# Kernel optimization log

Hardware: AMD Instinct MI355X
Metric: run time of the kernel (lower is better)

The kernel has to match this reference:

```python
import jax, jax.numpy as jnp
import numpy as np

EPS = 1e-12  # F.normalize eps


def setup_inputs() -> dict:
    key = jax.random.key(0)
    k1, k2, k3, k4 = jax.random.split(key, 4)
    D, K, H, W = 256, 64, 512, 512
    x = jax.random.normal(k1, (1, D, H, W), dtype=jnp.float32)
    c = jax.random.normal(k2, (K, D), dtype=jnp.float32)
    conv_w = jax.random.normal(k3, (K, D), dtype=jnp.float32) * (1.0 / np.sqrt(D))
    conv_b = jax.random.normal(k4, (K,), dtype=jnp.float32) * 0.01
    return {"x": x, "c": c, "conv_w": conv_w, "conv_b": conv_b}


def reference(x, c, conv_w, conv_b):
    # x: (1, D, H, W); base_cnn treated as identity (feature map given directly)
    _, D, H, W = x.shape
    K = conv_w.shape[0]
    N = H * W
    xf = x.reshape(D, N)                                  # (D, N) local descriptors

    # 1x1 conv soft-assignment: logits (K, N), softmax over clusters K
    logits = jnp.einsum('kd,dn->kn', conv_w, xf) + conv_b[:, None]
    a_bar = jax.nn.softmax(logits, axis=0)                # (K, N)

    # VLAD core (vectorized): V[k] = sum_n a_bar[k,n] * (x[:,n] - c[k])
    V = jnp.einsum('kn,dn->kd', a_bar, xf) - c * a_bar.sum(axis=1, keepdims=True)  # (K, D)

    # intra-normalization over cluster axis (dim=0), then per-row L2 (F.normalize default dim=1)
    V = V / jnp.maximum(jnp.linalg.norm(V, axis=0, keepdims=True), EPS)
    y = V / jnp.maximum(jnp.linalg.norm(V, axis=1, keepdims=True), EPS)
    return y
```

## Files before the change

kernel.cpp:

```cpp
#include <hip/hip_runtime.h>
#include <hip/hip_bf16.h>

#define DD    256
#define KK    64
#define NPIX  262144
#define NW    512
#define NWIN  2
#define GRID  256
#define BLOCK 1024

#define W_S   264
#define AB_S  520
#define XC_S  40
#define SV_S  129

typedef __attribute__((ext_vector_type(8))) short bf16x8;
typedef __attribute__((ext_vector_type(4))) float f32x4;

union Frag { bf16x8 v; int i[4]; };

__device__ __forceinline__ int cvtpk(float a, float b) {
    __hip_bfloat162 h = __float22bfloat162_rn(float2{a, b});
    int r; __builtin_memcpy(&r, &h, 4); return r;
}

__device__ __forceinline__ void lds_barrier() {
    asm volatile("s_waitcnt lgkmcnt(0)" ::: "memory");
    __builtin_amdgcn_s_barrier();
}

__global__ __launch_bounds__(BLOCK, 4)
void netvlad_fused(const float* __restrict__ x, const float* __restrict__ conv_w,
                   const float* __restrict__ conv_b, float* __restrict__ Vpart,
                   float* __restrict__ asum_part)
{
    __shared__ short Wl[KK * W_S];
    __shared__ short Ab[KK * AB_S];
    __shared__ union {
        short slice[16 * 32 * XC_S];
        float sv[KK * SV_S];
    } U2;

    const int t    = threadIdx.x;
    const int lane = t & 63;
    const int w    = t >> 6;
    const int l15  = lane & 15;
    const int q    = (lane >> 4) & 3;
    const int bid  = blockIdx.x;
    const size_t n0 = (size_t)bid * (NWIN * NW);

    const int dg = lane >> 3;
    const int ng = lane & 7;
    const size_t nself0 = n0 + 32 * w + 4 * ng;
    const size_t nself1 = n0 + NW + 32 * w + 4 * ng;

    float4 pr[2][4];
    #pragma unroll
    for (int j = 0; j < 4; ++j)
        pr[0][j] = *(const float4*)(x + (size_t)(4 * dg + j) * NPIX + nself0);
    __builtin_amdgcn_sched_barrier(0);

    #pragma unroll
    for (int i = 0; i < 16; ++i) {
        int idx = t + BLOCK * i;
        float wv = conv_w[idx];
        __hip_bfloat16 hb = __float2bfloat16(wv);
        short s; __builtin_memcpy(&s, &hb, 2);
        Wl[(idx >> 8) * W_S + (idx & 255)] = s;
    }

    #pragma unroll
    for (int j = 0; j < 4; ++j)
        pr[1][j] = *(const float4*)(x + (size_t)(32 + 4 * dg + j) * NPIX + nself0);
    __builtin_amdgcn_sched_barrier(0);

    lds_barrier();

    float asumReg = 0.f;
    f32x4 acc[4];
    #pragma unroll
    for (int ct = 0; ct < 4; ++ct) acc[ct] = (f32x4){0.f, 0.f, 0.f, 0.f};

    short* slice = &U2.slice[w * (32 * XC_S)];

    #pragma unroll
    for (int win = 0; win < NWIN; ++win) {
        const size_t nwin   = n0 + (size_t)win * NW;
        const size_t nselfw = nwin + 32 * w + 4 * ng;

        f32x4 Lc[2][4];
        #pragma unroll
        for (int nt = 0; nt < 2; ++nt)
            #pragma unroll
            for (int mt = 0; mt < 4; ++mt)
                Lc[nt][mt] = (f32x4){0.f, 0.f, 0.f, 0.f};

        #pragma unroll
        for (int ch = 0; ch < 8; ++ch) {
            const int cur = ch & 1;

            {
                const float* r0 = (const float*)&pr[cur][0];
                const float* r1 = (const float*)&pr[cur][1];
                const float* r2 = (const float*)&pr[cur][2];
                const float* r3 = (const float*)&pr[cur][3];
                #pragma unroll
                for (int c = 0; c < 4; ++c) {
                    int2 pk; pk.x = cvtpk(r0[c], r1[c]); pk.y = cvtpk(r2[c], r3[c]);
                    *(int2*)&slice[(4 * ng + c) * XC_S + 4 * dg] = pk;
                }
            }

            if (ch < 6) {
                #pragma unroll
                for (int j = 0; j < 4; ++j)
                    pr[cur][j] = *(const float4*)(x + (size_t)(32 * (ch + 2) + 4 * dg + j) * NPIX + nselfw);
                __builtin_amdgcn_sched_barrier(0);
            }

            Frag Bv[2];
            #pragma unroll
            for (int nt = 0; nt < 2; ++nt)
                Bv[nt] = *(const Frag*)&slice[(16 * nt + l15) * XC_S + 8 * q];
            #pragma unroll
            for (int mt = 0; mt < 4; ++mt) {
                Frag A = *(const Frag*)&Wl[(16 * mt + l15) * W_S + 32 * ch + 8 * q];
                #pragma unroll
                for (int nt = 0; nt < 2; ++nt)
                    Lc[nt][mt] = __builtin_amdgcn_mfma_f32_16x16x32_bf16(A.v, Bv[nt].v, Lc[nt][mt], 0, 0, 0);
            }
        }

        float breg[4][4];
        #pragma unroll
        for (int mt = 0; mt < 4; ++mt)
            #pragma unroll
            for (int r = 0; r < 4; ++r)
                breg[mt][r] = conv_b[16 * mt + 4 * q + r];

        #pragma unroll
        for (int nt = 0; nt < 2; ++nt) {
            float mx = -1e30f;
            #pragma unroll
            for (int mt = 0; mt < 4; ++mt)
                #pragma unroll
                for (int r = 0; r < 4; ++r) {
                    Lc[nt][mt][r] += breg[mt][r];
                    mx = fmaxf(mx, Lc[nt][mt][r]);
                }
            mx = fmaxf(mx, __shfl_xor(mx, 16));
            mx = fmaxf(mx, __shfl_xor(mx, 32));
            float s = 0.f;
            #pragma unroll
            for (int mt = 0; mt < 4; ++mt)
                #pragma unroll
                for (int r = 0; r < 4; ++r) {
                    float e = __expf(Lc[nt][mt][r] - mx);
                    Lc[nt][mt][r] = e;
                    s += e;
                }
            s += __shfl_xor(s, 16);
            s += __shfl_xor(s, 32);
            float inv = 1.0f / s;
            #pragma unroll
            for (int mt = 0; mt < 4; ++mt)
                #pragma unroll
                for (int r = 0; r < 4; ++r)
                    Lc[nt][mt][r] *= inv;
        }

        {
            float* buf = (float*)(U2.slice + w * (32 * XC_S));
            #pragma unroll
            for (int mt = 0; mt < 4; ++mt)
                #pragma unroll
                for (int r = 0; r < 4; ++r) {
                    float v = Lc[0][mt][r] + Lc[1][mt][r];
                    v += __shfl_xor(v, 1);
                    v += __shfl_xor(v, 2);
                    v += __shfl_xor(v, 4);
                    v += __shfl_xor(v, 8);
                    if (l15 == 0) buf[16 * mt + 4 * q + r] = v;
                }
        }

        #pragma unroll
        for (int nt = 0; nt < 2; ++nt)
            #pragma unroll
            for (int mt = 0; mt < 4; ++mt)
                #pragma unroll
                for (int r = 0; r < 4; ++r) {
                    __hip_bfloat16 hb = __float2bfloat16(Lc[nt][mt][r]);
                    short s; __builtin_memcpy(&s, &hb, 2);
                    Ab[(16 * mt + 4 * q + r) * AB_S + 32 * w + 16 * nt + l15] = s;
                }

        const float* xroww = x + (size_t)(16 * w + l15) * NPIX + nwin + 8 * q;
        float4 pv[4][2];
        #pragma unroll
        for (int d = 0; d < 4; ++d) {
            pv[d][0] = *(const float4*)(xroww + 32 * d);
            pv[d][1] = *(const float4*)(xroww + 32 * d + 4);
        }
        __builtin_amdgcn_sched_barrier(0);

        if (win == 0) {
            #pragma unroll
            for (int j = 0; j < 4; ++j)
                pr[0][j] = *(const float4*)(x + (size_t)(4 * dg + j) * NPIX + nself1);
            #pragma unroll
            for (int j = 0; j < 4; ++j)
                pr[1][j] = *(const float4*)(x + (size_t)(32 + 4 * dg + j) * NPIX + nself1);
            __builtin_amdgcn_sched_barrier(0);
        }

        lds_barrier();

        if (t < KK) {
            float s = 0.f;
            #pragma unroll
            for (int ww = 0; ww < 16; ++ww)
                s += ((const float*)(U2.slice + ww * (32 * XC_S)))[t];
            asumReg += s;
        }

        #pragma unroll
        for (int s = 0; s < 16; ++s) {
            const int cur = s & 3;
            Frag Af;
            Af.i[0] = cvtpk(pv[cur][0].x, pv[cur][0].y);
            Af.i[1] = cvtpk(pv[cur][0].z, pv[cur][0].w);
            Af.i[2] = cvtpk(pv[cur][1].x, pv[cur][1].y);
            Af.i[3] = cvtpk(pv[cur][1].z, pv[cur][1].w);
            if (s < 12) {
                pv[cur][0] = *(const float4*)(xroww + 32 * (s + 4));
                pv[cur][1] = *(const float4*)(xroww + 32 * (s + 4) + 4);
                __builtin_amdgcn_sched_barrier(0);
            }
            Frag Bf[4];
            #pragma unroll
            for (int ct = 0; ct < 4; ++ct)
                Bf[ct] = *(const Frag*)&Ab[(16 * ct + l15) * AB_S + 32 * s + 8 * q];
            #pragma unroll
            for (int ct = 0; ct < 4; ++ct)
                acc[ct] = __builtin_amdgcn_mfma_f32_16x16x32_bf16(Af.v, Bf[ct].v, acc[ct], 0, 0, 0);
        }

        if (win == 0)
            lds_barrier();
    }

    if (t < KK) asum_part[(size_t)bid * KK + t] = asumReg;

    float* vout = Vpart + (size_t)bid * (KK * DD);
    #pragma unroll
    for (int H = 0; H < 2; ++H) {
        __syncthreads();
        if ((w >> 3) == H) {
            #pragma unroll
            for (int ct = 0; ct < 4; ++ct)
                #pragma unroll
                for (int r = 0; r < 4; ++r) {
                    int k  = 16 * ct + l15;
                    int dl = 16 * w + 4 * q + r - 128 * H;
                    U2.sv[k * SV_S + dl] = acc[ct][r];
                }
        }
        __syncthreads();
        #pragma unroll
        for (int i = 0; i < 8; ++i) {
            int idx = t + BLOCK * i;
            int k = idx >> 7, dl = idx & 127;
            vout[k * DD + 128 * H + dl] = U2.sv[k * SV_S + dl];
        }
    }
}

__global__ __launch_bounds__(256)
void netvlad_reduce(const float* __restrict__ Vpart, const float* __restrict__ asum_part,
                    float* __restrict__ Vred, float* __restrict__ asum_red)
{
    __shared__ float sbuf[256];
    const int t = threadIdx.x;
    if (blockIdx.x < 256) {
        const int o = blockIdx.x * 64 + (t & 63);
        const int g = t >> 6;
        float s = 0.f;
        #pragma unroll 8
        for (int i = 0; i < 64; ++i)
            s += Vpart[(size_t)(g * 64 + i) * (KK * DD) + o];
        sbuf[t] = s;
        __syncthreads();
        if (t < 64) Vred[o] = sbuf[t] + sbuf[t + 64] + sbuf[t + 128] + sbuf[t + 192];
    } else {
        const int k = t & 63;
        const int g = t >> 6;
        float s = 0.f;
        #pragma unroll 8
        for (int i = 0; i < 64; ++i)
            s += asum_part[(size_t)(g * 64 + i) * KK + k];
        sbuf[t] = s;
        __syncthreads();
        if (t < 64) asum_red[k] = sbuf[t] + sbuf[t + 64] + sbuf[t + 128] + sbuf[t + 192];
    }
}

__global__ __launch_bounds__(1024)
void netvlad_finalize(const float* __restrict__ Vws, const float* __restrict__ asum_ws,
                      const float* __restrict__ c, float* __restrict__ y)
{
    __shared__ float sV[KK * DD];
    __shared__ float sa[KK];
    __shared__ float colf[DD];
    __shared__ float rowf[KK];
    const int t = threadIdx.x;

    if (t < KK) sa[t] = asum_ws[t];
    __syncthreads();

    #pragma unroll
    for (int i = 0; i < 16; ++i) {
        int idx = t + 1024 * i;
        sV[idx] = Vws[idx] - c[idx] * sa[idx >> 8];
    }
    __syncthreads();

    if (t < DD) {
        float s = 0.f;
        for (int k = 0; k < KK; ++k) { float v = sV[k * DD + t]; s += v * v; }
        colf[t] = 1.0f / fmaxf(sqrtf(s), 1e-12f);
    }
    __syncthreads();

    #pragma unroll
    for (int i = 0; i < 16; ++i) {
        int idx = t + 1024 * i;
        sV[idx] *= colf[idx & 255];
    }
    __syncthreads();

    {
        int k = t >> 4, p = t & 15;
        float s = 0.f;
        #pragma unroll
        for (int j = 0; j < 16; ++j) { float v = sV[k * DD + p + 16 * j]; s += v * v; }
        s += __shfl_xor(s, 1);
        s += __shfl_xor(s, 2);
        s += __shfl_xor(s, 4);
        s += __shfl_xor(s, 8);
        if (p == 0) rowf[k] = 1.0f / fmaxf(sqrtf(s), 1e-12f);
    }
    __syncthreads();

    #pragma unroll
    for (int i = 0; i < 16; ++i) {
        int idx = t + 1024 * i;
        y[idx] = sV[idx] * rowf[idx >> 8];
    }
}

extern "C" void kernel_launch(void* const* d_in, const int* in_sizes, int n_in,
                              void* d_out, int out_size, void* d_ws, size_t ws_size,
                              hipStream_t stream) {
    const float* x      = (const float*)d_in[0];
    const float* c      = (const float*)d_in[1];
    const float* conv_w = (const float*)d_in[2];
    const float* conv_b = (const float*)d_in[3];
    float* y = (float*)d_out;

    float* Vpart     = (float*)d_ws;
    float* asum_part = Vpart + (size_t)GRID * KK * DD;
    float* Vred      = asum_part + (size_t)GRID * KK;
    float* asum_red  = Vred + KK * DD;

    netvlad_fused<<<GRID, BLOCK, 0, stream>>>(x, conv_w, conv_b, Vpart, asum_part);
    netvlad_reduce<<<257, 256, 0, stream>>>(Vpart, asum_part, Vred, asum_red);
    netvlad_finalize<<<1, 1024, 0, stream>>>(Vred, asum_red, c, y);
}
```

Baseline: 101.4 us.

## Split waves into producer/consumer roles with double-buffered soft-assignment tiles

Waves 0-7 now compute logits and softmax for a 256-pixel window, and waves 8-15 accumulate the VLAD product for the previous window out of a double-buffered Ab tile. The intent is to overlap the assignment GEMM and softmax with the aggregation GEMM, where before each wave ran both phases in sequence with barriers between them. Each window now costs one barrier instead of two serialized phases. In exchange, consumer waves hold twice as many accumulators and the pipeline takes one extra fill step. The two halves may also be unequal in work, which would leave some waves idle.

```diff
diff --git a/kernel.cpp b/kernel.cpp
--- a/kernel.cpp
+++ b/kernel.cpp
@@ -4,13 +4,13 @@
 #define DD    256
 #define KK    64
 #define NPIX  262144
-#define NW    512
-#define NWIN  2
+#define NW    256
+#define NWIN  4
 #define GRID  256
 #define BLOCK 1024
 
 #define W_S   264
-#define AB_S  520
+#define AB_S  264
 #define XC_S  40
 #define SV_S  129
 
@@ -35,9 +35,10 @@
                    float* __restrict__ asum_part)
 {
     __shared__ short Wl[KK * W_S];
-    __shared__ short Ab[KK * AB_S];
+    __shared__ short Ab[2][KK * AB_S];
+    __shared__ float asb[2][8][KK];
     __shared__ union {
-        short slice[16 * 32 * XC_S];
+        short slice[8 * 32 * XC_S];
         float sv[KK * SV_S];
     } U2;
 
@@ -49,16 +50,20 @@
     const int bid  = blockIdx.x;
     const size_t n0 = (size_t)bid * (NWIN * NW);
 
+    const bool producer = (w < 8);
+    const int  cw = w - 8;
+
     const int dg = lane >> 3;
     const int ng = lane & 7;
     const size_t nself0 = n0 + 32 * w + 4 * ng;
-    const size_t nself1 = n0 + NW + 32 * w + 4 * ng;
 
     float4 pr[2][4];
-    #pragma unroll
-    for (int j = 0; j < 4; ++j)
-        pr[0][j] = *(const float4*)(x + (size_t)(4 * dg + j) * NPIX + nself0);
-    __builtin_amdgcn_sched_barrier(0);
+    if (producer) {
+        #pragma unroll
+        for (int j = 0; j < 4; ++j)
+            pr[0][j] = *(const float4*)(x + (size_t)(4 * dg + j) * NPIX + nself0);
+        __builtin_amdgcn_sched_barrier(0);
+    }
 
     #pragma unroll
     for (int i = 0; i < 16; ++i) {
@@ -69,207 +74,220 @@
         Wl[(idx >> 8) * W_S + (idx & 255)] = s;
     }
 
-    #pragma unroll
-    for (int j = 0; j < 4; ++j)
-        pr[1][j] = *(const float4*)(x + (size_t)(32 + 4 * dg + j) * NPIX + nself0);
-    __builtin_amdgcn_sched_barrier(0);
+    if (producer) {
+        #pragma unroll
+        for (int j = 0; j < 4; ++j)
+            pr[1][j] = *(const float4*)(x + (size_t)(32 + 4 * dg + j) * NPIX + nself0);
+        __builtin_amdgcn_sched_barrier(0);
+    }
+
+    f32x4 acc[2][4];
+    #pragma unroll
+    for (int rg = 0; rg < 2; ++rg)
+        #pragma unroll
+        for (int ct = 0; ct < 4; ++ct)
+            acc[rg][ct] = (f32x4){0.f, 0.f, 0.f, 0.f};
+    float asumReg = 0.f;
 
     lds_barrier();
 
-    float asumReg = 0.f;
-    f32x4 acc[4];
-    #pragma unroll
-    for (int ct = 0; ct < 4; ++ct) acc[ct] = (f32x4){0.f, 0.f, 0.f, 0.f};
-
-    short* slice = &U2.slice[w * (32 * XC_S)];
-
-    #pragma unroll
-    for (int win = 0; win < NWIN; ++win) {
-        const size_t nwin   = n0 + (size_t)win * NW;
-        const size_t nselfw = nwin + 32 * w + 4 * ng;
-
-        f32x4 Lc[2][4];
-        #pragma unroll
-        for (int nt = 0; nt < 2; ++nt)
-            #pragma unroll
-            for (int mt = 0; mt < 4; ++mt)
-                Lc[nt][mt] = (f32x4){0.f, 0.f, 0.f, 0.f};
-
-        #pragma unroll
-        for (int ch = 0; ch < 8; ++ch) {
-            const int cur = ch & 1;
-
-            {
-                const float* r0 = (const float*)&pr[cur][0];
-                const float* r1 = (const float*)&pr[cur][1];
-                const float* r2 = (const float*)&pr[cur][2];
-                const float* r3 = (const float*)&pr[cur][3];
-                #pragma unroll
-                for (int c = 0; c < 4; ++c) {
-                    int2 pk; pk.x = cvtpk(r0[c], r1[c]); pk.y = cvtpk(r2[c], r3[c]);
-                    *(int2*)&slice[(4 * ng + c) * XC_S + 4 * dg] = pk;
-                }
+    for (int i = 0; i <= NWIN; ++i) {
+        if (producer) {
+            if (i < NWIN) {
+                const size_t nwin   = n0 + (size_t)i * NW;
+                const size_t nselfw = nwin + 32 * w + 4 * ng;
+                short* slice = &U2.slice[w * (32 * XC_S)];
+
+                f32x4 Lc[2][4];
+                #pragma unroll
+                for (int nt = 0; nt < 2; ++nt)
+                    #pragma unroll
+                    for (int mt = 0; mt < 4; ++mt)
+                        Lc[nt][mt] = (f32x4){0.f, 0.f, 0.f, 0.f};
+
+                #pragma unroll
+                for (int ch = 0; ch < 8; ++ch) {
+                    const int cur = ch & 1;
+
+                    {
+                        const float* r0 = (const float*)&pr[cur][0];
+                        const float* r1 = (const float*)&pr[cur][1];
+                        const float* r2 = (const float*)&pr[cur][2];
+                        const float* r3 = (const float*)&pr[cur][3];
+                        #pragma unroll
+                        for (int c = 0; c < 4; ++c) {
+                            int2 pk; pk.x = cvtpk(r0[c], r1[c]); pk.y = cvtpk(r2[c], r3[c]);
+                            *(int2*)&slice[(4 * ng + c) * XC_S + 4 * dg] = pk;
+                        }
+                    }
+
+                    if (ch < 6) {
+                        #pragma unroll
+                        for (int j = 0; j < 4; ++j)
+                            pr[cur][j] = *(const float4*)(x + (size_t)(32 * (ch + 2) + 4 * dg + j) * NPIX + nselfw);
+                        __builtin_amdgcn_sched_barrier(0);
+                    }
+                    if (ch == 7 && i + 1 < NWIN) {
+                        const size_t nselfn = nselfw + NW;
+                        #pragma unroll
+                        for (int j = 0; j < 4; ++j)
+                            pr[0][j] = *(const float4*)(x + (size_t)(4 * dg + j) * NPIX + nselfn);
+                        #pragma unroll
+                        for (int j = 0; j < 4; ++j)
+                            pr[1][j] = *(const float4*)(x + (size_t)(32 + 4 * dg + j) * NPIX + nselfn);
+                        __builtin_amdgcn_sched_barrier(0);
+                    }
+
+                    Frag Bv[2];
+                    #pragma unroll
+                    for (int nt = 0; nt < 2; ++nt)
+                        Bv[nt] = *(const Frag*)&slice[(16 * nt + l15) * XC_S + 8 * q];
+                    #pragma unroll
+                    for (int mt = 0; mt < 4; ++mt) {
+                        Frag A = *(const Frag*)&Wl[(16 * mt + l15) * W_S + 32 * ch + 8 * q];
+                        #pragma unroll
+                        for (int nt = 0; nt < 2; ++nt)
+                            Lc[nt][mt] = __builtin_amdgcn_mfma_f32_16x16x32_bf16(A.v, Bv[nt].v, Lc[nt][mt], 0, 0, 0);
+                    }
+                }
+
+                #pragma unroll
+                for (int nt = 0; nt < 2; ++nt) {
+                    float mx = -1e30f;
+                    #pragma unroll
+                    for (int mt = 0; mt < 4; ++mt)
+                        #pragma unroll
+                        for (int r = 0; r < 4; ++r) {
+                            Lc[nt][mt][r] += conv_b[16 * mt + 4 * q + r];
+                            mx = fmaxf(mx, Lc[nt][mt][r]);
+                        }
+                    mx = fmaxf(mx, __shfl_xor(mx, 16));
+                    mx = fmaxf(mx, __shfl_xor(mx, 32));
+                    float s = 0.f;
+                    #pragma unroll
+                    for (int mt = 0; mt < 4; ++mt)
+                        #pragma unroll
+                        for (int r = 0; r < 4; ++r) {
+                            float e = __expf(Lc[nt][mt][r] - mx);
+                            Lc[nt][mt][r] = e;
+                            s += e;
+                        }
+                    s += __shfl_xor(s, 16);
+                    s += __shfl_xor(s, 32);
+                    float inv = 1.0f / s;
+                    #pragma unroll
+                    for (int mt = 0; mt < 4; ++mt)
+                        #pragma unroll
+                        for (int r = 0; r < 4; ++r)
+                            Lc[nt][mt][r] *= inv;
+                }
+
+                #pragma unroll
+                for (int mt = 0; mt < 4; ++mt)
+                    #pragma unroll
+                    for (int r = 0; r < 4; ++r) {
+                        float v = Lc[0][mt][r] + Lc[1][mt][r];
+                        v += __shfl_xor(v, 1);
+                        v += __shfl_xor(v, 2);
+                        v += __shfl_xor(v, 4);
+                        v += __shfl_xor(v, 8);
+                        if (l15 == 0) asb[i & 1][w][16 * mt + 4 * q + r] = v;
+                    }
+
+                #pragma unroll
+                for (int nt = 0; nt < 2; ++nt)
+                    #pragma unroll
+                    for (int mt = 0; mt < 4; ++mt)
+                        #pragma unroll
+                        for (int r = 0; r < 4; ++r) {
+                            __hip_bfloat16 hb = __float2bfloat16(Lc[nt][mt][r]);
+                            short s; __builtin_memcpy(&s, &hb, 2);
+                            Ab[i & 1][(16 * mt + 4 * q + r) * AB_S + 32 * w + 16 * nt + l15] = s;
+                        }
             }
-
-            if (ch < 6) {
-                #pragma unroll
-                for (int j = 0; j < 4; ++j)
-                    pr[cur][j] = *(const float4*)(x + (size_t)(32 * (ch + 2) + 4 * dg + j) * NPIX + nselfw);
+        } else {
+            if (i > 0) {
+                const int win = i - 1;
+                const size_t nwin = n0 + (size_t)win * NW;
+                const short* ab = Ab[win & 1];
+                const float* xr0 = x + (size_t)(32 * cw + l15) * NPIX + nwin + 8 * q;
+                const float* xr1 = xr0 + (size_t)16 * NPIX;
+
+                float4 pv[2][2][2];
+                #pragma unroll
+                for (int d = 0; d < 2; ++d) {
+                    pv[d][0][0] = *(const float4*)(xr0 + 32 * d);
+                    pv[d][0][1] = *(const float4*)(xr0 + 32 * d + 4);
+                    pv[d][1][0] = *(const float4*)(xr1 + 32 * d);
+                    pv[d][1][1] = *(const float4*)(xr1 + 32 * d + 4);
+                }
                 __builtin_amdgcn_sched_barrier(0);
-            }
-
-            Frag Bv[2];
-            #pragma unroll
-            for (int nt = 0; nt < 2; ++nt)
-                Bv[nt] = *(const Frag*)&slice[(16 * nt + l15) * XC_S + 8 * q];
-            #pragma unroll
-            for (int mt = 0; mt < 4; ++mt) {
-                Frag A = *(const Frag*)&Wl[(16 * mt + l15) * W_S + 32 * ch + 8 * q];
-                #pragma unroll
-                for (int nt = 0; nt < 2; ++nt)
-                    Lc[nt][mt] = __builtin_amdgcn_mfma_f32_16x16x32_bf16(A.v, Bv[nt].v, Lc[nt][mt], 0, 0, 0);
+
+                #pragma unroll
+                for (int s = 0; s < 8; ++s) {
+                    const int cur = s & 1;
+                    Frag Af[2];
+                    #pragma unroll
+                    for (int rg = 0; rg < 2; ++rg) {
+                        Af[rg].i[0] = cvtpk(pv[cur][rg][0].x, pv[cur][rg][0].y);
+                        Af[rg].i[1] = cvtpk(pv[cur][rg][0].z, pv[cur][rg][0].w);
+                        Af[rg].i[2] = cvtpk(pv[cur][rg][1].x, pv[cur][rg][1].y);
+                        Af[rg].i[3] = cvtpk(pv[cur][rg][1].z, pv[cur][rg][1].w);
+                    }
+                    if (s < 6) {
+                        pv[cur][0][0] = *(const float4*)(xr0 + 32 * (s + 2));
+                        pv[cur][0][1] = *(const float4*)(xr0 + 32 * (s + 2) + 4);
+                        pv[cur][1][0] = *(const float4*)(xr1 + 32 * (s + 2));
+                        pv[cur][1][1] = *(const float4*)(xr1 + 32 * (s + 2) + 4);
+                        __builtin_amdgcn_sched_barrier(0);
+                    }
+                    Frag Bf[4];
+                    #pragma unroll
+                    for (int ct = 0; ct < 4; ++ct)
+                        Bf[ct] = *(const Frag*)&ab[(16 * ct + l15) * AB_S + 32 * s + 8 * q];
+                    #pragma unroll
+                    for (int ct = 0; ct < 4; ++ct) {
+                        acc[0][ct] = __builtin_amdgcn_mfma_f32_16x16x32_bf16(Af[0].v, Bf[ct].v, acc[0][ct], 0, 0, 0);
+                        acc[1][ct] = __builtin_amdgcn_mfma_f32_16x16x32_bf16(Af[1].v, Bf[ct].v, acc[1][ct], 0, 0, 0);
+                    }
+                }
+
+                if (w == 8) {
+                    #pragma unroll
+                    for (int pp = 0; pp < 8; ++pp)
+                        asumReg += asb[win & 1][pp][lane];
+                }
             }
         }
-
-        float breg[4][4];
-        #pragma unroll
-        for (int mt = 0; mt < 4; ++mt)
-            #pragma unroll
-            for (int r = 0; r < 4; ++r)
-                breg[mt][r] = conv_b[16 * mt + 4 * q + r];
-
-        #pragma unroll
-        for (int nt = 0; nt < 2; ++nt) {
-            float mx = -1e30f;
-            #pragma unroll
-            for (int mt = 0; mt < 4; ++mt)
-                #pragma unroll
-                for (int r = 0; r < 4; ++r) {
-                    Lc[nt][mt][r] += breg[mt][r];
-                    mx = fmaxf(mx, Lc[nt][mt][r]);
-                }
-            mx = fmaxf(mx, __shfl_xor(mx, 16));
-            mx = fmaxf(mx, __shfl_xor(mx, 32));
-            float s = 0.f;
-            #pragma unroll
-            for (int mt = 0; mt < 4; ++mt)
-                #pragma unroll
-                for (int r = 0; r < 4; ++r) {
-                    float e = __expf(Lc[nt][mt][r] - mx);
-                    Lc[nt][mt][r] = e;
-                    s += e;
-                }
-            s += __shfl_xor(s, 16);
-            s += __shfl_xor(s, 32);
-            float inv = 1.0f / s;
-            #pragma unroll
-            for (int mt = 0; mt < 4; ++mt)
-                #pragma unroll
-                for (int r = 0; r < 4; ++r)
-                    Lc[nt][mt][r] *= inv;
-        }
-
-        {
-            float* buf = (float*)(U2.slice + w * (32 * XC_S));
-            #pragma unroll
-            for (int mt = 0; mt < 4; ++mt)
-                #pragma unroll
-                for (int r = 0; r < 4; ++r) {
-                    float v = Lc[0][mt][r] + Lc[1][mt][r];
-                    v += __shfl_xor(v, 1);
-                    v += __shfl_xor(v, 2);
-                    v += __shfl_xor(v, 4);
-                    v += __shfl_xor(v, 8);
-                    if (l15 == 0) buf[16 * mt + 4 * q + r] = v;
-                }
-        }
-
-        #pragma unroll
-        for (int nt = 0; nt < 2; ++nt)
-            #pragma unroll
-            for (int mt = 0; mt < 4; ++mt)
-                #pragma unroll
-                for (int r = 0; r < 4; ++r) {
-                    __hip_bfloat16 hb = __float2bfloat16(Lc[nt][mt][r]);
-                    short s; __builtin_memcpy(&s, &hb, 2);
-                    Ab[(16 * mt + 4 * q + r) * AB_S + 32 * w + 16 * nt + l15] = s;
-                }
-
-        const float* xroww = x + (size_t)(16 * w + l15) * NPIX + nwin + 8 * q;
-        float4 pv[4][2];
-        #pragma unroll
-        for (int d = 0; d < 4; ++d) {
-            pv[d][0] = *(const float4*)(xroww + 32 * d);
-            pv[d][1] = *(const float4*)(xroww + 32 * d + 4);
-        }
-        __builtin_amdgcn_sched_barrier(0);
-
-        if (win == 0) {
-            #pragma unroll
-            for (int j = 0; j < 4; ++j)
-                pr[0][j] = *(const float4*)(x + (size_t)(4 * dg + j) * NPIX + nself1);
-            #pragma unroll
-            for (int j = 0; j < 4; ++j)
-                pr[1][j] = *(const float4*)(x + (size_t)(32 + 4 * dg + j) * NPIX + nself1);
-            __builtin_amdgcn_sched_barrier(0);
-        }
-
         lds_barrier();
-
-        if (t < KK) {
-            float s = 0.f;
-            #pragma unroll
-            for (int ww = 0; ww < 16; ++ww)
-                s += ((const float*)(U2.slice + ww * (32 * XC_S)))[t];
-            asumReg += s;
-        }
-
-        #pragma unroll
-        for (int s = 0; s < 16; ++s) {
-            const int cur = s & 3;
-            Frag Af;
-            Af.i[0] = cvtpk(pv[cur][0].x, pv[cur][0].y);
-            Af.i[1] = cvtpk(pv[cur][0].z, pv[cur][0].w);
-            Af.i[2] = cvtpk(pv[cur][1].x, pv[cur][1].y);
-            Af.i[3] = cvtpk(pv[cur][1].z, pv[cur][1].w);
-            if (s < 12) {
-                pv[cur][0] = *(const float4*)(xroww + 32 * (s + 4));
-                pv[cur][1] = *(const float4*)(xroww + 32 * (s + 4) + 4);
-                __builtin_amdgcn_sched_barrier(0);
-            }
-            Frag Bf[4];
-            #pragma unroll
-            for (int ct = 0; ct < 4; ++ct)
-                Bf[ct] = *(const Frag*)&Ab[(16 * ct + l15) * AB_S + 32 * s + 8 * q];
-            #pragma unroll
-            for (int ct = 0; ct < 4; ++ct)
-                acc[ct] = __builtin_amdgcn_mfma_f32_16x16x32_bf16(Af.v, Bf[ct].v, acc[ct], 0, 0, 0);
-        }
-
-        if (win == 0)
-            lds_barrier();
-    }
-
-    if (t < KK) asum_part[(size_t)bid * KK + t] = asumReg;
+    }
+
+    if (w == 8) asum_part[(size_t)bid * KK + lane] = asumReg;
 
     float* vout = Vpart + (size_t)bid * (KK * DD);
     #pragma unroll
     for (int H = 0; H < 2; ++H) {
         __syncthreads();
-        if ((w >> 3) == H) {
+        if (!producer) {
             #pragma unroll
-            for (int ct = 0; ct < 4; ++ct)
-                #pragma unroll
-                for (int r = 0; r < 4; ++r) {
-                    int k  = 16 * ct + l15;
-                    int dl = 16 * w + 4 * q + r - 128 * H;
-                    U2.sv[k * SV_S + dl] = acc[ct][r];
-                }
+            for (int rg = 0; rg < 2; ++rg) {
+                const int dbase = 32 * cw + 16 * rg;
+                if ((dbase >> 7) == H) {
+                    #pragma unroll
+                    for (int ct = 0; ct < 4; ++ct)
+                        #pragma unroll
+                        for (int r = 0; r < 4; ++r) {
+                            int k  = 16 * ct + l15;
+                            int dl = dbase + 4 * q + r - 128 * H;
+                            U2.sv[k * SV_S + dl] = acc[rg][ct][r];
+                        }
+                }
+            }
         }
         __syncthreads();
         #pragma unroll
-        for (int i = 0; i < 8; ++i) {
-            int idx = t + BLOCK * i;
+        for (int ii = 0; ii < 8; ++ii) {
+            int idx = t + BLOCK * ii;
             int k = idx >> 7, dl = idx & 127;
             vout[k * DD + 128 * H + dl] = U2.sv[k * SV_S + dl];
         }
```

Measured after the change: 149.9 us. 47.8% more time.

## Software-pipeline logits and VLAD GEMMs across smaller double-buffered windows

Applied to the files above, without the earlier changes.

The pixel window is halved and the number of windows doubled. The loop is restructured so that iteration i computes the logits and softmax for window i while running the VLAD accumulation MFMAs for window i-1, using double-buffered assignment and column-sum LDS buffers. This removes the per-window serialisation between the two GEMM phases and one barrier per window, so the matrix and memory work of both stages can overlap. The cost is more LDS for the double buffers, an extra loop iteration of prologue/epilogue work, and more register pressure under the fixed occupancy target.

```diff
diff --git a/kernel.cpp b/kernel.cpp
--- a/kernel.cpp
+++ b/kernel.cpp
@@ -4,13 +4,13 @@
 #define DD    256
 #define KK    64
 #define NPIX  262144
-#define NW    512
-#define NWIN  2
+#define NW    256
+#define NWIN  4
 #define GRID  256
 #define BLOCK 1024
 
 #define W_S   264
-#define AB_S  520
+#define AB_S  264
 #define XC_S  40
 #define SV_S  129
 
@@ -29,15 +29,16 @@
     __builtin_amdgcn_s_barrier();
 }
 
-__global__ __launch_bounds__(BLOCK, 4)
+__global__ __attribute__((amdgpu_flat_work_group_size(BLOCK, BLOCK), amdgpu_waves_per_eu(4, 4)))
 void netvlad_fused(const float* __restrict__ x, const float* __restrict__ conv_w,
                    const float* __restrict__ conv_b, float* __restrict__ Vpart,
                    float* __restrict__ asum_part)
 {
     __shared__ short Wl[KK * W_S];
-    __shared__ short Ab[KK * AB_S];
+    __shared__ short Ab[2][KK * AB_S];
+    __shared__ float asb[2][16][KK];
     __shared__ union {
-        short slice[16 * 32 * XC_S];
+        short slice[16 * 16 * XC_S];
         float sv[KK * SV_S];
     } U2;
 
@@ -49,15 +50,16 @@
     const int bid  = blockIdx.x;
     const size_t n0 = (size_t)bid * (NWIN * NW);
 
-    const int dg = lane >> 3;
-    const int ng = lane & 7;
-    const size_t nself0 = n0 + 32 * w + 4 * ng;
-    const size_t nself1 = n0 + NW + 32 * w + 4 * ng;
-
-    float4 pr[2][4];
-    #pragma unroll
-    for (int j = 0; j < 4; ++j)
-        pr[0][j] = *(const float4*)(x + (size_t)(4 * dg + j) * NPIX + nself0);
+    const int p  = lane >> 2;
+    const int ng = lane & 3;
+    const size_t nself0 = n0 + 16 * w + 4 * ng;
+
+    const float* xrow_base = x + (size_t)(16 * w + l15) * NPIX + n0 + 8 * q;
+
+    float4 pr[2][2];
+    #pragma unroll
+    for (int j = 0; j < 2; ++j)
+        pr[0][j] = *(const float4*)(x + (size_t)(2 * p + j) * NPIX + nself0);
     __builtin_amdgcn_sched_barrier(0);
 
     #pragma unroll
@@ -70,83 +72,96 @@
     }
 
     #pragma unroll
-    for (int j = 0; j < 4; ++j)
-        pr[1][j] = *(const float4*)(x + (size_t)(32 + 4 * dg + j) * NPIX + nself0);
+    for (int j = 0; j < 2; ++j)
+        pr[1][j] = *(const float4*)(x + (size_t)(32 + 2 * p + j) * NPIX + nself0);
     __builtin_amdgcn_sched_barrier(0);
 
+    f32x4 acc[4];
+    #pragma unroll
+    for (int ct = 0; ct < 4; ++ct) acc[ct] = (f32x4){0.f, 0.f, 0.f, 0.f};
+    float asumReg = 0.f;
+    float4 pv[2][2];
+
     lds_barrier();
 
-    float asumReg = 0.f;
-    f32x4 acc[4];
-    #pragma unroll
-    for (int ct = 0; ct < 4; ++ct) acc[ct] = (f32x4){0.f, 0.f, 0.f, 0.f};
-
-    short* slice = &U2.slice[w * (32 * XC_S)];
-
-    #pragma unroll
-    for (int win = 0; win < NWIN; ++win) {
-        const size_t nwin   = n0 + (size_t)win * NW;
-        const size_t nselfw = nwin + 32 * w + 4 * ng;
-
-        f32x4 Lc[2][4];
+    for (int i = 0; i <= NWIN; ++i) {
+        const int ib = i & 1;
+        const int pb = ib ^ 1;
+
+        if (i > 0 && t < KK) {
+            float s = 0.f;
+            #pragma unroll
+            for (int ww = 0; ww < 16; ++ww) s += asb[pb][ww][t];
+            asumReg += s;
+        }
+
+        const size_t nwin   = n0 + (size_t)i * NW;
+        const size_t nselfw = nwin + 16 * w + 4 * ng;
+        const float* xroww  = xrow_base + (size_t)(i - 1) * NW;
+        short* slice = &U2.slice[w * (16 * XC_S)];
+
+        f32x4 Lc[4];
         #pragma unroll
-        for (int nt = 0; nt < 2; ++nt)
-            #pragma unroll
-            for (int mt = 0; mt < 4; ++mt)
-                Lc[nt][mt] = (f32x4){0.f, 0.f, 0.f, 0.f};
+        for (int mt = 0; mt < 4; ++mt) Lc[mt] = (f32x4){0.f, 0.f, 0.f, 0.f};
 
         #pragma unroll
         for (int ch = 0; ch < 8; ++ch) {
             const int cur = ch & 1;
 
-            {
+            if (i < NWIN) {
                 const float* r0 = (const float*)&pr[cur][0];
                 const float* r1 = (const float*)&pr[cur][1];
-                const float* r2 = (const float*)&pr[cur][2];
-                const float* r3 = (const float*)&pr[cur][3];
                 #pragma unroll
                 for (int c = 0; c < 4; ++c) {
-                    int2 pk; pk.x = cvtpk(r0[c], r1[c]); pk.y = cvtpk(r2[c], r3[c]);
-                    *(int2*)&slice[(4 * ng + c) * XC_S + 4 * dg] = pk;
-                }
-            }
-
-            if (ch < 6) {
-                #pragma unroll
-                for (int j = 0; j < 4; ++j)
-                    pr[cur][j] = *(const float4*)(x + (size_t)(32 * (ch + 2) + 4 * dg + j) * NPIX + nselfw);
-                __builtin_amdgcn_sched_barrier(0);
-            }
-
-            Frag Bv[2];
-            #pragma unroll
-            for (int nt = 0; nt < 2; ++nt)
-                Bv[nt] = *(const Frag*)&slice[(16 * nt + l15) * XC_S + 8 * q];
-            #pragma unroll
-            for (int mt = 0; mt < 4; ++mt) {
-                Frag A = *(const Frag*)&Wl[(16 * mt + l15) * W_S + 32 * ch + 8 * q];
-                #pragma unroll
-                for (int nt = 0; nt < 2; ++nt)
-                    Lc[nt][mt] = __builtin_amdgcn_mfma_f32_16x16x32_bf16(A.v, Bv[nt].v, Lc[nt][mt], 0, 0, 0);
-            }
-        }
-
-        float breg[4][4];
-        #pragma unroll
-        for (int mt = 0; mt < 4; ++mt)
-            #pragma unroll
-            for (int r = 0; r < 4; ++r)
-                breg[mt][r] = conv_b[16 * mt + 4 * q + r];
-
-        #pragma unroll
-        for (int nt = 0; nt < 2; ++nt) {
+                    int pk = cvtpk(r0[c], r1[c]);
+                    *(int*)&slice[(4 * ng + c) * XC_S + 2 * p] = pk;
+                }
+                if (ch < 6) {
+                    #pragma unroll
+                    for (int j = 0; j < 2; ++j)
+                        pr[cur][j] = *(const float4*)(x + (size_t)(32 * (ch + 2) + 2 * p + j) * NPIX + nselfw);
+                    __builtin_amdgcn_sched_barrier(0);
+                }
+            }
+
+            if (i > 0) {
+                Frag Af;
+                Af.i[0] = cvtpk(pv[cur][0].x, pv[cur][0].y);
+                Af.i[1] = cvtpk(pv[cur][0].z, pv[cur][0].w);
+                Af.i[2] = cvtpk(pv[cur][1].x, pv[cur][1].y);
+                Af.i[3] = cvtpk(pv[cur][1].z, pv[cur][1].w);
+                if (ch < 6) {
+                    pv[cur][0] = *(const float4*)(xroww + 32 * (ch + 2));
+                    pv[cur][1] = *(const float4*)(xroww + 32 * (ch + 2) + 4);
+                    __builtin_amdgcn_sched_barrier(0);
+                }
+                Frag Bf[4];
+                #pragma unroll
+                for (int ct = 0; ct < 4; ++ct)
+                    Bf[ct] = *(const Frag*)&Ab[pb][(16 * ct + l15) * AB_S + 32 * ch + 8 * q];
+                #pragma unroll
+                for (int ct = 0; ct < 4; ++ct)
+                    acc[ct] = __builtin_amdgcn_mfma_f32_16x16x32_bf16(Af.v, Bf[ct].v, acc[ct], 0, 0, 0);
+            }
+
+            if (i < NWIN) {
+                Frag Bv = *(const Frag*)&slice[l15 * XC_S + 8 * q];
+                #pragma unroll
+                for (int mt = 0; mt < 4; ++mt) {
+                    Frag A = *(const Frag*)&Wl[(16 * mt + l15) * W_S + 32 * ch + 8 * q];
+                    Lc[mt] = __builtin_amdgcn_mfma_f32_16x16x32_bf16(A.v, Bv.v, Lc[mt], 0, 0, 0);
+                }
+            }
+        }
+
+        if (i < NWIN) {
             float mx = -1e30f;
             #pragma unroll
             for (int mt = 0; mt < 4; ++mt)
                 #pragma unroll
                 for (int r = 0; r < 4; ++r) {
-                    Lc[nt][mt][r] += breg[mt][r];
-                    mx = fmaxf(mx, Lc[nt][mt][r]);
+                    Lc[mt][r] += conv_b[16 * mt + 4 * q + r];
+                    mx = fmaxf(mx, Lc[mt][r]);
                 }
             mx = fmaxf(mx, __shfl_xor(mx, 16));
             mx = fmaxf(mx, __shfl_xor(mx, 32));
@@ -155,8 +170,8 @@
             for (int mt = 0; mt < 4; ++mt)
                 #pragma unroll
                 for (int r = 0; r < 4; ++r) {
-                    float e = __expf(Lc[nt][mt][r] - mx);
-                    Lc[nt][mt][r] = e;
+                    float e = __expf(Lc[mt][r] - mx);
+                    Lc[mt][r] = e;
                     s += e;
                 }
             s += __shfl_xor(s, 16);
@@ -166,88 +181,52 @@
             for (int mt = 0; mt < 4; ++mt)
                 #pragma unroll
                 for (int r = 0; r < 4; ++r)
-                    Lc[nt][mt][r] *= inv;
-        }
-
-        {
-            float* buf = (float*)(U2.slice + w * (32 * XC_S));
-            #pragma unroll
-            for (int mt = 0; mt < 4; ++mt)
-                #pragma unroll
-                for (int r = 0; r < 4; ++r) {
-                    float v = Lc[0][mt][r] + Lc[1][mt][r];
+                    Lc[mt][r] *= inv;
+
+            #pragma unroll
+            for (int mt = 0; mt < 4; ++mt)
+                #pragma unroll
+                for (int r = 0; r < 4; ++r) {
+                    float v = Lc[mt][r];
                     v += __shfl_xor(v, 1);
                     v += __shfl_xor(v, 2);
                     v += __shfl_xor(v, 4);
                     v += __shfl_xor(v, 8);
-                    if (l15 == 0) buf[16 * mt + 4 * q + r] = v;
-                }
-        }
-
-        #pragma unroll
-        for (int nt = 0; nt < 2; ++nt)
-            #pragma unroll
-            for (int mt = 0; mt < 4; ++mt)
-                #pragma unroll
-                for (int r = 0; r < 4; ++r) {
-                    __hip_bfloat16 hb = __float2bfloat16(Lc[nt][mt][r]);
-                    short s; __builtin_memcpy(&s, &hb, 2);
-                    Ab[(16 * mt + 4 * q + r) * AB_S + 32 * w + 16 * nt + l15] = s;
-                }
-
-        const float* xroww = x + (size_t)(16 * w + l15) * NPIX + nwin + 8 * q;
-        float4 pv[4][2];
-        #pragma unroll
-        for (int d = 0; d < 4; ++d) {
-            pv[d][0] = *(const float4*)(xroww + 32 * d);
-            pv[d][1] = *(const float4*)(xroww + 32 * d + 4);
-        }
-        __builtin_amdgcn_sched_barrier(0);
-
-        if (win == 0) {
-            #pragma unroll
-            for (int j = 0; j < 4; ++j)
-                pr[0][j] = *(const float4*)(x + (size_t)(4 * dg + j) * NPIX + nself1);
-            #pragma unroll
-            for (int j = 0; j < 4; ++j)
-                pr[1][j] = *(const float4*)(x + (size_t)(32 + 4 * dg + j) * NPIX + nself1);
-            __builtin_amdgcn_sched_barrier(0);
+                    if (l15 == 0) asb[ib][w][16 * mt + 4 * q + r] = v;
+                }
+
+            #pragma unroll
+            for (int mt = 0; mt < 4; ++mt)
+                #pragma unroll
+                for (int r = 0; r < 4; ++r) {
+                    __hip_bfloat16 hb = __float2bfloat16(Lc[mt][r]);
+                    short sv_; __builtin_memcpy(&sv_, &hb, 2);
+                    Ab[ib][(16 * mt + 4 * q + r) * AB_S + 16 * w + l15] = sv_;
+                }
+
+            if (i + 1 < NWIN) {
+                const size_t nselfn = nselfw + NW;
+                #pragma unroll
+                for (int j = 0; j < 2; ++j)
+                    pr[0][j] = *(const float4*)(x + (size_t)(2 * p + j) * NPIX + nselfn);
+                #pragma unroll
+                for (int j = 0; j < 2; ++j)
+                    pr[1][j] = *(const float4*)(x + (size_t)(32 + 2 * p + j) * NPIX + nselfn);
+                __builtin_amdgcn_sched_barrier(0);
+            }
+
+            {
+                const float* xnext = xrow_base + (size_t)i * NW;
+                #pragma unroll
+                for (int d = 0; d < 2; ++d) {
+                    pv[d][0] = *(const float4*)(xnext + 32 * d);
+                    pv[d][1] = *(const float4*)(xnext + 32 * d + 4);
+                }
+                __builtin_amdgcn_sched_barrier(0);
+            }
         }
 
         lds_barrier();
-
-        if (t < KK) {
-            float s = 0.f;
-            #pragma unroll
-            for (int ww = 0; ww < 16; ++ww)
-                s += ((const float*)(U2.slice + ww * (32 * XC_S)))[t];
-            asumReg += s;
-        }
-
-        #pragma unroll
-        for (int s = 0; s < 16; ++s) {
-            const int cur = s & 3;
-            Frag Af;
-            Af.i[0] = cvtpk(pv[cur][0].x, pv[cur][0].y);
-            Af.i[1] = cvtpk(pv[cur][0].z, pv[cur][0].w);
-            Af.i[2] = cvtpk(pv[cur][1].x, pv[cur][1].y);
-            Af.i[3] = cvtpk(pv[cur][1].z, pv[cur][1].w);
-            if (s < 12) {
-                pv[cur][0] = *(const float4*)(xroww + 32 * (s + 4));
-                pv[cur][1] = *(const float4*)(xroww + 32 * (s + 4) + 4);
-                __builtin_amdgcn_sched_barrier(0);
-            }
-            Frag Bf[4];
-            #pragma unroll
-            for (int ct = 0; ct < 4; ++ct)
-                Bf[ct] = *(const Frag*)&Ab[(16 * ct + l15) * AB_S + 32 * s + 8 * q];
-            #pragma unroll
-            for (int ct = 0; ct < 4; ++ct)
-                acc[ct] = __builtin_amdgcn_mfma_f32_16x16x32_bf16(Af.v, Bf[ct].v, acc[ct], 0, 0, 0);
-        }
-
-        if (win == 0)
-            lds_barrier();
     }
 
     if (t < KK) asum_part[(size_t)bid * KK + t] = asumReg;
@@ -268,8 +247,8 @@
         }
         __syncthreads();
         #pragma unroll
-        for (int i = 0; i < 8; ++i) {
-            int idx = t + BLOCK * i;
+        for (int ii = 0; ii < 8; ++ii) {
+            int idx = t + BLOCK * ii;
             int k = idx >> 7, dl = idx & 127;
             vout[k * DD + 128 * H + dl] = U2.sv[k * SV_S + dl];
         }
```

After: 106.1 us. +4.6%, slower.
